# Kernel tuning notes

Measured on AMD Instinct MI355X. Metric: run time of the kernel, lower is better.

The kernel has to match this reference:

```python
import jax, jax.numpy as jnp
import numpy as np

D_MODEL = 1024
D_STATE = 16
EXPAND = 2
D_HEAD = 64
D_CONV = 4
FFN = 2816
NORMALIZE_BC = True
D_INNER = EXPAND * D_MODEL          # 2048
N_HEADS = D_INNER // D_HEAD         # 32
EPS = 1e-6


def _rmsnorm(x, w):
    v = jnp.mean(x * x, axis=-1, keepdims=True)
    return x * jax.lax.rsqrt(v + EPS) * w


def _mixer(x, in_proj_w, conv_w, conv_b, A_log, dt_bias, D, out_proj_w):
    b, l, _ = x.shape
    zxbcdt = x @ in_proj_w.T  # (b, l, 2*D_INNER + 2*D_STATE + N_HEADS)
    z, xBC, dt_raw = jnp.split(zxbcdt, [D_INNER, 2 * D_INNER + 2 * D_STATE], axis=-1)
    # causal depthwise conv over (u, B, C) channels
    xp = jnp.pad(xBC, ((0, 0), (D_CONV - 1, 0), (0, 0)))
    y = conv_b + sum(xp[:, k:k + l, :] * conv_w[:, k] for k in range(D_CONV))
    xBC = jax.nn.silu(y)
    u, Bm, Cm = jnp.split(xBC, [D_INNER, D_INNER + D_STATE], axis=-1)
    if NORMALIZE_BC:
        Bm = Bm / (jnp.linalg.norm(Bm, axis=-1, keepdims=True) + EPS)
        Cm = Cm / (jnp.linalg.norm(Cm, axis=-1, keepdims=True) + EPS)
    dt = jax.nn.softplus(dt_raw + dt_bias)          # (b, l, h)
    A = jnp.exp(A_log)                              # (h, n) oscillator frequencies >= 0
    u = u.reshape(b, l, N_HEADS, D_HEAD)

    # LinOSS implicit (IM) discretization of z' = -A y + B u ; y' = z
    #   S  = 1/(1 + dt^2 A)
    #   w_k = S*(w_{k-1} - dt*A*y_{k-1} + dt*B u_k)
    #   y_k = y_{k-1} + dt*w_k ;  out_k = C y_k + D u_k
    def step(carry, inp):
        w, ys = carry                               # each (b, h, dh, n)
        dt_t, B_t, C_t, u_t = inp                   # (b,h),(b,n),(b,n),(b,h,dh)
        S = 1.0 / (1.0 + (dt_t[:, :, None] ** 2) * A[None])   # (b,h,n)
        Sb = S[:, :, None, :]
        dtb = dt_t[:, :, None, None]
        Ab = A[None, :, None, :]
        Bu = B_t[:, None, None, :] * u_t[..., None]            # (b,h,dh,n)
        w = Sb * (w - dtb * Ab * ys + dtb * Bu)
        ys = ys + dtb * w
        o = jnp.einsum('bhdn,bn->bhd', ys, C_t)
        return (w, ys), o

    init = (jnp.zeros((b, N_HEADS, D_HEAD, D_STATE), x.dtype),
            jnp.zeros((b, N_HEADS, D_HEAD, D_STATE), x.dtype))
    xs = (dt.transpose(1, 0, 2), Bm.transpose(1, 0, 2),
          Cm.transpose(1, 0, 2), u.transpose(1, 0, 2, 3))
    _, ys = jax.lax.scan(step, init, xs)            # (l, b, h, dh)
    ys = ys.transpose(1, 0, 2, 3) + D[None, None, :, None] * u
    out = ys.reshape(b, l, D_INNER) * jax.nn.silu(z)
    return out @ out_proj_w.T


def setup_inputs() -> dict:
    key = jax.random.key(0)
    ks = jax.random.split(key, 12)
    B, L = 4, 2048
    proj_dim = 2 * D_INNER + 2 * D_STATE + N_HEADS
    conv_ch = D_INNER + 2 * D_STATE
    s = lambda k, shape, sc: jax.random.normal(k, shape, jnp.float32) * sc
    return {
        "x": s(ks[0], (B, L, D_MODEL), 1.0),
        "norm1_w": jnp.ones((D_MODEL,), jnp.float32),
        "in_proj_w": s(ks[1], (proj_dim, D_MODEL), D_MODEL ** -0.5),
        "conv_w": s(ks[2], (conv_ch, D_CONV), 0.3),
        "conv_b": jnp.zeros((conv_ch,), jnp.float32),
        "A_log": s(ks[3], (N_HEADS, D_STATE), 0.5),
        "dt_bias": s(ks[4], (N_HEADS,), 0.5),
        "D": s(ks[5], (N_HEADS,), 1.0),
        "out_proj_w": s(ks[6], (D_MODEL, D_INNER), D_INNER ** -0.5),
        "norm2_w": jnp.ones((D_MODEL,), jnp.float32),
        "gate_w": s(ks[7], (FFN, D_MODEL), D_MODEL ** -0.5),
        "up_w": s(ks[8], (FFN, D_MODEL), D_MODEL ** -0.5),
        "down_w": s(ks[9], (D_MODEL, FFN), FFN ** -0.5),
    }


def reference(x, norm1_w, in_proj_w, conv_w, conv_b, A_log, dt_bias, D,
              out_proj_w, norm2_w, gate_w, up_w, down_w):
    h = x + _mixer(_rmsnorm(x, norm1_w), in_proj_w, conv_w, conv_b,
                   A_log, dt_bias, D, out_proj_w)
    hn = _rmsnorm(h, norm2_w)
    ffn = (jax.nn.silu(hn @ gate_w.T) * (hn @ up_w.T)) @ down_w.T
    return h + ffn
```

## Files before the change

kernel.cpp:

```cpp
#include <hip/hip_runtime.h>
#include <hip/hip_bf16.h>

#define D_MODEL   1024
#define D_STATE   16
#define D_HEAD    64
#define D_CONV    4
#define FFN_DIM   2816
#define D_INNER   2048
#define N_HEADS   32
#define BATCH     4
#define SEQ       2048
#define ROWS      (BATCH*SEQ)
#define PROJ_DIM  4160
#define ZX_N      4096
#define CH        128
#define NCH       (SEQ/CH)
#define GU_N      5632

typedef __bf16 bf16x8 __attribute__((ext_vector_type(8)));
typedef float  f32x4  __attribute__((ext_vector_type(4)));
typedef float  f32x2  __attribute__((ext_vector_type(2)));

__device__ __forceinline__ float siluf(float x) { return x / (1.0f + __expf(-x)); }

#define SBAR() do { asm volatile("" ::: "memory"); __builtin_amdgcn_s_barrier(); asm volatile("" ::: "memory"); } while (0)
#define LGKM0() asm volatile("s_waitcnt lgkmcnt(0)" ::: "memory")
#define VMCNT4() asm volatile("s_waitcnt vmcnt(4)" ::: "memory")
#define VMCNT2() asm volatile("s_waitcnt vmcnt(2)" ::: "memory")
#define VMCNT0() asm volatile("s_waitcnt vmcnt(0)" ::: "memory")

__global__ void cvt_k(const float* __restrict__ src, __hip_bfloat16* __restrict__ dst, int n) {
  int i = blockIdx.x * blockDim.x + threadIdx.x;
  if (i < n) dst[i] = __float2bfloat16(src[i]);
}

__global__ void cvt_gu_k(const float* __restrict__ wg, const float* __restrict__ wu,
                         __hip_bfloat16* __restrict__ dst) {
  int i = blockIdx.x * blockDim.x + threadIdx.x;
  if (i >= GU_N * D_MODEL) return;
  int r = i >> 10, c = i & 1023;
  int tile = r >> 8, rr = r & 255;
  const float* src = (rr < 128)
      ? wg + (size_t)(tile * 128 + rr) * D_MODEL + c
      : wu + (size_t)(tile * 128 + (rr - 128)) * D_MODEL + c;
  dst[i] = __float2bfloat16(*src);
}

__global__ __launch_bounds__(256) void rmsnorm_k(const float* __restrict__ x,
                                                 const float* __restrict__ w,
                                                 __hip_bfloat16* __restrict__ out,
                                                 float* __restrict__ outf) {
  int row = blockIdx.x;
  int t = threadIdx.x;
  const float* xr = x + (size_t)row * D_MODEL;
  float4 v = ((const float4*)xr)[t];
  float ss = v.x*v.x + v.y*v.y + v.z*v.z + v.w*v.w;
  #pragma unroll
  for (int o = 32; o > 0; o >>= 1) ss += __shfl_xor(ss, o);
  __shared__ float red[4];
  if ((t & 63) == 0) red[t >> 6] = ss;
  __syncthreads();
  ss = red[0] + red[1] + red[2] + red[3];
  float scale = rsqrtf(ss * (1.0f / D_MODEL) + 1e-6f);
  float4 wv = ((const float4*)w)[t];
  float4 r;
  r.x = v.x * scale * wv.x; r.y = v.y * scale * wv.y;
  r.z = v.z * scale * wv.z; r.w = v.w * scale * wv.w;
  __hip_bfloat16* orow = out + (size_t)row * D_MODEL + t * 4;
  orow[0] = __float2bfloat16(r.x);
  orow[1] = __float2bfloat16(r.y);
  orow[2] = __float2bfloat16(r.z);
  orow[3] = __float2bfloat16(r.w);
  if (outf) ((float4*)(outf + (size_t)row * D_MODEL))[t] = r;
}

__global__ __launch_bounds__(256) void vecproj_k(const float* __restrict__ xn,
                                                 const float* __restrict__ wi,
                                                 const float* __restrict__ dtb,
                                                 float* __restrict__ dtT,
                                                 float* __restrict__ bcraw) {
  const int r0 = blockIdx.x * 4;
  const int t  = threadIdx.x;
  const int o   = t >> 2;
  const int seg = t & 3;

  __shared__ float xs[4][D_MODEL];
  #pragma unroll
  for (int i = 0; i < 4; ++i)
    ((float4*)&xs[i][0])[t] = ((const float4*)(xn + (size_t)(r0 + i) * D_MODEL))[t];
  __syncthreads();

  const int wrow = (o < 32) ? (2 * D_INNER + o) : (2 * D_INNER + 2 * D_STATE + (o - 32));
  const float4* w4 = (const float4*)(wi + (size_t)wrow * D_MODEL) + seg * 64;
  const float4* x0 = (const float4*)&xs[0][0] + seg * 64;
  const float4* x1 = (const float4*)&xs[1][0] + seg * 64;
  const float4* x2 = (const float4*)&xs[2][0] + seg * 64;
  const float4* x3 = (const float4*)&xs[3][0] + seg * 64;
  float a0 = 0.f, a1 = 0.f, a2 = 0.f, a3 = 0.f;
  #pragma unroll 8
  for (int k = 0; k < 64; ++k) {
    float4 wv = w4[k];
    float4 v0 = x0[k], v1 = x1[k], v2 = x2[k], v3 = x3[k];
    a0 = fmaf(wv.x, v0.x, fmaf(wv.y, v0.y, fmaf(wv.z, v0.z, fmaf(wv.w, v0.w, a0))));
    a1 = fmaf(wv.x, v1.x, fmaf(wv.y, v1.y, fmaf(wv.z, v1.z, fmaf(wv.w, v1.w, a1))));
    a2 = fmaf(wv.x, v2.x, fmaf(wv.y, v2.y, fmaf(wv.z, v2.z, fmaf(wv.w, v2.w, a2))));
    a3 = fmaf(wv.x, v3.x, fmaf(wv.y, v3.y, fmaf(wv.z, v3.z, fmaf(wv.w, v3.w, a3))));
  }
  #pragma unroll
  for (int m = 1; m < 4; m <<= 1) {
    a0 += __shfl_xor(a0, m);
    a1 += __shfl_xor(a1, m);
    a2 += __shfl_xor(a2, m);
    a3 += __shfl_xor(a3, m);
  }
  if (seg == 0) {
    float v[4] = {a0, a1, a2, a3};
    if (o < 32) {
      #pragma unroll
      for (int i = 0; i < 4; ++i) bcraw[(size_t)(r0 + i) * 32 + o] = v[i];
    } else {
      int hh = o - 32;
      float bias = dtb[hh];
      #pragma unroll
      for (int i = 0; i < 4; ++i) {
        float xv = v[i] + bias;
        dtT[(size_t)hh * ROWS + r0 + i] = (xv > 20.f) ? xv : log1pf(__expf(xv));
      }
    }
  }
}

template<int EPI>
__global__ __launch_bounds__(512, 2) void gemm8(
    const __hip_bfloat16* __restrict__ A,
    const __hip_bfloat16* __restrict__ Bw,
    float* __restrict__ Cf,
    __hip_bfloat16* __restrict__ Cb,
    const float* __restrict__ add_src,
    int M, int N, int K)
{
  extern __shared__ char lds[];
  const int nwg = (M >> 8) * (N >> 8);
  int bid = blockIdx.x;
  bid = (bid & 7) * (nwg >> 3) + (bid >> 3);
  const int ntn = N >> 8;
  const int bm = (bid / ntn) << 8;
  const int bn = (bid % ntn) << 8;

  const int tid  = threadIdx.x;
  const int wid  = tid >> 6;
  const int lane = tid & 63;
  const int wm = wid >> 2;
  const int wn = wid & 3;
  const int r16 = lane & 15;
  const int kg  = lane >> 4;

  const int rb = ((r16 << 6) + (kg << 4)) ^ ((r16 & 8) << 2);

  const int s_sub = tid >> 6;
  const int s_w   = (tid & 63) << 4;
  const int s_wp  = s_w ^ ((((s_w) >> 9) & 1) << 5);
  const int s_row = ((s_sub >> 1) << 4) + (s_wp >> 6);
  const int s_col = ((s_sub & 1) << 5) + ((s_wp >> 1) & 31);

  auto stage = [&](int buf, int mat, int half, int c, int kt) {
    const __hip_bfloat16* src = (mat == 0)
        ? A  + (size_t)(bm + half * 128 + c * 64 + s_row) * K + kt * 64 + s_col
        : Bw + (size_t)(bn + half * 128 + c * 64 + s_row) * K + kt * 64 + s_col;
    char* dst = lds + buf * 65536 + mat * 32768 + half * 16384 + c * 8192 + tid * 16;
    __builtin_amdgcn_global_load_lds((const __attribute__((address_space(1))) unsigned int*)src,
                                     (__attribute__((address_space(3))) unsigned int*)dst,
                                     16, 0, 0);
  };

  f32x4 acc[8][4] = {};
  bf16x8 af[4][2], bfr[4][2];

  const int NT = K >> 6;
  stage(0,0,0,0,0); stage(0,0,0,1,0); stage(0,0,1,0,0); stage(0,0,1,1,0);
  stage(0,1,0,0,0); stage(0,1,0,1,0); stage(0,1,1,0,0); stage(0,1,1,1,0);
  __syncthreads();

  for (int kt = 0; kt < NT; ++kt) {
    const int buf = kt & 1, nbuf = buf ^ 1;
    const bool st = (kt + 1 < NT);
    const char* Ab = lds + buf * 65536 + wm * 16384;
    const char* Bb = lds + buf * 65536 + 32768 + (wn >> 1) * 16384 + (wn & 1) * 8192;

    #pragma unroll
    for (int mi2 = 0; mi2 < 4; ++mi2)
      #pragma unroll
      for (int kk = 0; kk < 2; ++kk)
        af[mi2][kk] = *(const bf16x8*)(Ab + (mi2 * 2 + kk) * 1024 + rb);
    #pragma unroll
    for (int ni = 0; ni < 2; ++ni)
      #pragma unroll
      for (int kk = 0; kk < 2; ++kk)
        bfr[ni][kk] = *(const bf16x8*)(Bb + (ni * 2 + kk) * 1024 + rb);
    if (st) { stage(nbuf,1,0,0,kt+1); stage(nbuf,1,0,1,kt+1); }
    SBAR(); LGKM0();
    __builtin_amdgcn_s_setprio(1);
    #pragma unroll
    for (int mi2 = 0; mi2 < 4; ++mi2)
      #pragma unroll
      for (int ni = 0; ni < 2; ++ni)
        #pragma unroll
        for (int kk = 0; kk < 2; ++kk)
          acc[mi2][ni] = __builtin_amdgcn_mfma_f32_16x16x32_bf16(af[mi2][kk], bfr[ni][kk], acc[mi2][ni], 0, 0, 0);
    __builtin_amdgcn_s_setprio(0);
    SBAR();

    #pragma unroll
    for (int ni = 2; ni < 4; ++ni)
      #pragma unroll
      for (int kk = 0; kk < 2; ++kk)
        bfr[ni][kk] = *(const bf16x8*)(Bb + (ni * 2 + kk) * 1024 + rb);
    if (st) { stage(nbuf,1,1,0,kt+1); stage(nbuf,1,1,1,kt+1); }
    SBAR(); LGKM0();
    __builtin_amdgcn_s_setprio(1);
    #pragma unroll
    for (int mi2 = 0; mi2 < 4; ++mi2)
      #pragma unroll
      for (int ni = 2; ni < 4; ++ni)
        #pragma unroll
        for (int kk = 0; kk < 2; ++kk)
          acc[mi2][ni] = __builtin_amdgcn_mfma_f32_16x16x32_bf16(af[mi2][kk], bfr[ni][kk], acc[mi2][ni], 0, 0, 0);
    __builtin_amdgcn_s_setprio(0);
    if (st) { VMCNT4(); } else { VMCNT0(); }
    SBAR();

    #pragma unroll
    for (int mi2 = 0; mi2 < 4; ++mi2)
      #pragma unroll
      for (int kk = 0; kk < 2; ++kk)
        af[mi2][kk] = *(const bf16x8*)(Ab + ((4 + mi2) * 2 + kk) * 1024 + rb);
    if (st) { stage(nbuf,0,0,0,kt+1); stage(nbuf,0,1,0,kt+1); }
    SBAR(); LGKM0();
    __builtin_amdgcn_s_setprio(1);
    #pragma unroll
    for (int mi2 = 0; mi2 < 4; ++mi2)
      #pragma unroll
      for (int ni = 0; ni < 2; ++ni)
        #pragma unroll
        for (int kk = 0; kk < 2; ++kk)
          acc[4 + mi2][ni] = __builtin_amdgcn_mfma_f32_16x16x32_bf16(af[mi2][kk], bfr[ni][kk], acc[4 + mi2][ni], 0, 0, 0);
    __builtin_amdgcn_s_setprio(0);
    SBAR();

    if (st) { stage(nbuf,0,0,1,kt+1); stage(nbuf,0,1,1,kt+1); }
    SBAR(); LGKM0();
    __builtin_amdgcn_s_setprio(1);
    #pragma unroll
    for (int mi2 = 0; mi2 < 4; ++mi2)
      #pragma unroll
      for (int ni = 2; ni < 4; ++ni)
        #pragma unroll
        for (int kk = 0; kk < 2; ++kk)
          acc[4 + mi2][ni] = __builtin_amdgcn_mfma_f32_16x16x32_bf16(af[mi2][kk], bfr[ni][kk], acc[4 + mi2][ni], 0, 0, 0);
    __builtin_amdgcn_s_setprio(0);
    VMCNT2();
    SBAR();
  }

  if constexpr (EPI == 4) {
    float* xch = (float*)lds;
    __syncthreads();
    if (wn < 2) {
      #pragma unroll
      for (int mi = 0; mi < 8; ++mi)
        #pragma unroll
        for (int ni = 0; ni < 4; ++ni)
          #pragma unroll
          for (int j = 0; j < 4; ++j) {
            int row = mi * 16 + kg * 4 + j;
            int col = wn * 64 + ni * 16 + r16;
            int cc = col ^ (((row >> 2) & 1) << 4);
            xch[wm * 16384 + row * 128 + cc] = siluf(acc[mi][ni][j]);
          }
    }
    __syncthreads();
    if (wn >= 2) {
      #pragma unroll
      for (int mi = 0; mi < 8; ++mi)
        #pragma unroll
        for (int ni = 0; ni < 4; ++ni)
          #pragma unroll
          for (int j = 0; j < 4; ++j) {
            int row = mi * 16 + kg * 4 + j;
            int col = (wn - 2) * 64 + ni * 16 + r16;
            int cc = col ^ (((row >> 2) & 1) << 4);
            float g = xch[wm * 16384 + row * 128 + cc];
            int r = bm + wm * 128 + row;
            int tc = (bn >> 1) + col;
            Cb[(size_t)r * FFN_DIM + tc] = __float2bfloat16(g * acc[mi][ni][j]);
          }
    }
  } else {
    #pragma unroll
    for (int mi = 0; mi < 8; ++mi) {
      #pragma unroll
      for (int ni = 0; ni < 4; ++ni) {
        #pragma unroll
        for (int j = 0; j < 4; ++j) {
          int r = bm + wm * 128 + mi * 16 + kg * 4 + j;
          int c = bn + wn * 64 + ni * 16 + r16;
          size_t idx = (size_t)r * N + c;
          float v = acc[mi][ni][j];
          if constexpr (EPI == 0) {
            Cf[idx] = v;
          } else if constexpr (EPI == 1) {
            Cf[idx] = v + add_src[idx];
          } else if constexpr (EPI == 5) {
            Cb[idx] = __float2bfloat16(v);
          }
        }
      }
    }
  }
}

template<int EPI>
__global__ __launch_bounds__(512, 2) void gemm8B(
    const __hip_bfloat16* __restrict__ A,
    const __hip_bfloat16* __restrict__ Bw,
    float* __restrict__ Cf,
    __hip_bfloat16* __restrict__ Cb,
    const float* __restrict__ add_src,
    int M, int N, int K)
{
  extern __shared__ char lds[];
  const int nwg = (M >> 8) * (N >> 7);
  int bid = blockIdx.x;
  bid = (bid & 7) * (nwg >> 3) + (bid >> 3);
  const int ntn = N >> 7;
  const int bm = (bid / ntn) << 8;
  const int bn = (bid % ntn) << 7;

  const int tid  = threadIdx.x;
  const int wid  = tid >> 6;
  const int lane = tid & 63;
  const int wm = wid >> 2;
  const int wn = wid & 3;
  const int r16 = lane & 15;
  const int kg  = lane >> 4;

  const int rb = ((r16 << 6) + (kg << 4)) ^ ((r16 & 8) << 2);

  const int s_sub = tid >> 6;
  const int s_w   = (tid & 63) << 4;
  const int s_wp  = s_w ^ ((((s_w) >> 9) & 1) << 5);
  const int s_row = ((s_sub >> 1) << 4) + (s_wp >> 6);
  const int s_col = ((s_sub & 1) << 5) + ((s_wp >> 1) & 31);

  auto stageA = [&](int buf, int half, int c, int kt) {
    const __hip_bfloat16* src = A + (size_t)(bm + half * 128 + c * 64 + s_row) * K + kt * 64 + s_col;
    char* dst = lds + buf * 65536 + half * 16384 + c * 8192 + tid * 16;
    __builtin_amdgcn_global_load_lds((const __attribute__((address_space(1))) unsigned int*)src,
                                     (__attribute__((address_space(3))) unsigned int*)dst,
                                     16, 0, 0);
  };
  auto stageB = [&](int buf, int c, int kt) {
    const __hip_bfloat16* src = Bw + (size_t)(bn + c * 64 + s_row) * K + kt * 64 + s_col;
    char* dst = lds + buf * 65536 + 32768 + c * 8192 + tid * 16;
    __builtin_amdgcn_global_load_lds((const __attribute__((address_space(1))) unsigned int*)src,
                                     (__attribute__((address_space(3))) unsigned int*)dst,
                                     16, 0, 0);
  };

  f32x4 acc[8][2] = {};
  bf16x8 af[4][2], bfr[2][2];

  const int NT = K >> 6;
  stageB(0,0,0); stageB(0,1,0);
  stageA(0,0,0,0); stageA(0,1,0,0); stageA(0,0,1,0); stageA(0,1,1,0);
  __syncthreads();

  for (int kt = 0; kt < NT; ++kt) {
    const int buf = kt & 1, nbuf = buf ^ 1;
    const bool st = (kt + 1 < NT);
    const char* Ab = lds + buf * 65536 + wm * 16384;
    const char* Bb = lds + buf * 65536 + 32768 + (wn >> 1) * 8192 + (wn & 1) * 4096;

    #pragma unroll
    for (int mi2 = 0; mi2 < 4; ++mi2)
      #pragma unroll
      for (int kk = 0; kk < 2; ++kk)
        af[mi2][kk] = *(const bf16x8*)(Ab + (mi2 * 2 + kk) * 1024 + rb);
    #pragma unroll
    for (int ni = 0; ni < 2; ++ni)
      #pragma unroll
      for (int kk = 0; kk < 2; ++kk)
        bfr[ni][kk] = *(const bf16x8*)(Bb + (ni * 2 + kk) * 1024 + rb);
    if (st) { stageB(nbuf,0,kt+1); stageB(nbuf,1,kt+1); stageA(nbuf,0,0,kt+1); stageA(nbuf,1,0,kt+1); }
    SBAR(); LGKM0();
    __builtin_amdgcn_s_setprio(1);
    #pragma unroll
    for (int mi2 = 0; mi2 < 4; ++mi2)
      #pragma unroll
      for (int ni = 0; ni < 2; ++ni)
        #pragma unroll
        for (int kk = 0; kk < 2; ++kk)
          acc[mi2][ni] = __builtin_amdgcn_mfma_f32_16x16x32_bf16(af[mi2][kk], bfr[ni][kk], acc[mi2][ni], 0, 0, 0);
    __builtin_amdgcn_s_setprio(0);
    if (st) { VMCNT4(); } else { VMCNT0(); }
    SBAR();

    #pragma unroll
    for (int mi2 = 0; mi2 < 4; ++mi2)
      #pragma unroll
      for (int kk = 0; kk < 2; ++kk)
        af[mi2][kk] = *(const bf16x8*)(Ab + ((4 + mi2) * 2 + kk) * 1024 + rb);
    if (st) { stageA(nbuf,0,1,kt+1); stageA(nbuf,1,1,kt+1); }
    SBAR(); LGKM0();
    __builtin_amdgcn_s_setprio(1);
    #pragma unroll
    for (int mi2 = 0; mi2 < 4; ++mi2)
      #pragma unroll
      for (int ni = 0; ni < 2; ++ni)
        #pragma unroll
        for (int kk = 0; kk < 2; ++kk)
          acc[4 + mi2][ni] = __builtin_amdgcn_mfma_f32_16x16x32_bf16(af[mi2][kk], bfr[ni][kk], acc[4 + mi2][ni], 0, 0, 0);
    __builtin_amdgcn_s_setprio(0);
    VMCNT2();
    SBAR();
  }

  #pragma unroll
  for (int mi = 0; mi < 8; ++mi) {
    #pragma unroll
    for (int ni = 0; ni < 2; ++ni) {
      #pragma unroll
      for (int j = 0; j < 4; ++j) {
        int r = bm + wm * 128 + mi * 16 + kg * 4 + j;
        int c = bn + wn * 32 + ni * 16 + r16;
        size_t idx = (size_t)r * N + c;
        float v = acc[mi][ni][j];
        if constexpr (EPI == 0) {
          Cf[idx] = v;
        } else if constexpr (EPI == 1) {
          Cf[idx] = v + add_src[idx];
        }
      }
    }
  }
}

__global__ __launch_bounds__(256) void duconv_k(const __hip_bfloat16* __restrict__ zxb,
                                                const float* __restrict__ cw,
                                                const float* __restrict__ cb,
                                                __hip_bfloat16* __restrict__ u_po) {
  int idx = blockIdx.x * 256 + threadIdx.x;
  int q = idx & 511;
  int r = idx >> 9;
  int d0 = q << 2;
  int l = r & (SEQ - 1);
  float4 cb4 = ((const float4*)cb)[q];
  float tw[4][4];
  #pragma unroll
  for (int i = 0; i < 4; ++i) {
    float4 t = ((const float4*)cw)[d0 + i];
    tw[i][0] = t.x; tw[i][1] = t.y; tw[i][2] = t.z; tw[i][3] = t.w;
  }
  float a[4] = {cb4.x, cb4.y, cb4.z, cb4.w};
  #pragma unroll
  for (int k = 0; k < 4; ++k) {
    if (l - 3 + k >= 0) {
      union { ushort4 u4; __hip_bfloat16 b[4]; } R;
      R.u4 = *(const ushort4*)(zxb + (size_t)(r - 3 + k) * ZX_N + D_INNER + d0);
      a[0] = fmaf(__bfloat162float(R.b[0]), tw[0][k], a[0]);
      a[1] = fmaf(__bfloat162float(R.b[1]), tw[1][k], a[1]);
      a[2] = fmaf(__bfloat162float(R.b[2]), tw[2][k], a[2]);
      a[3] = fmaf(__bfloat162float(R.b[3]), tw[3][k], a[3]);
    }
  }
  union { ushort4 u4; __hip_bfloat16 b[4]; } pk;
  #pragma unroll
  for (int i = 0; i < 4; ++i) pk.b[i] = __float2bfloat16(siluf(a[i]));
  *(ushort4*)(u_po + (size_t)r * D_INNER + d0) = pk.u4;
}

__global__ __launch_bounds__(256) void bcdt_k(const float* __restrict__ bcraw,
                                              const float* __restrict__ cw,
                                              const float* __restrict__ cb,
                                              float* __restrict__ bc) {
  int t = threadIdx.x;
  int r = blockIdx.x * 8 + (t >> 5);
  int ch = t & 31;
  int l = r & (SEQ - 1);
  int c = D_INNER + ch;
  float acc = cb[c];
  #pragma unroll
  for (int k = 0; k < 4; ++k) {
    int lp = l - 3 + k;
    if (lp >= 0)
      acc = fmaf(bcraw[(size_t)(r - 3 + k) * 32 + ch], cw[c * 4 + k], acc);
  }
  acc = siluf(acc);
  float ss = acc * acc;
  ss += __shfl_xor(ss, 1);
  ss += __shfl_xor(ss, 2);
  ss += __shfl_xor(ss, 4);
  ss += __shfl_xor(ss, 8);
  bc[r * 32 + ch] = acc / (sqrtf(ss) + 1e-6f);
}

__global__ __launch_bounds__(256) void pk_k(const float* __restrict__ dtT,
                                            const float* __restrict__ A_log,
                                            float* __restrict__ Pm) {
  int bh = blockIdx.x;
  int h = bh & 31;
  int t = threadIdx.x;
  int ch = t >> 4, n = t & 15;
  float a = __expf(A_log[h * 16 + n]);
  const float* dtp = dtT + (size_t)h * ROWS + (size_t)(bh >> 5) * SEQ + ch * CH;
  float p00 = 1.f, p01 = 0.f, p10 = 0.f, p11 = 1.f;
  for (int l = 0; l < CH; ++l) {
    float dt = dtp[l];
    float s  = 1.0f / fmaf(dt * dt, a, 1.0f);
    float m00 = s;
    float m01 = -dt * a * s;
    float m10 = dt * s;
    float m11 = fmaf(-dt * a, m10, 1.0f);
    float q00 = fmaf(m00, p00, m01 * p10);
    float q01 = fmaf(m00, p01, m01 * p11);
    float q10 = fmaf(m10, p00, m11 * p10);
    float q11 = fmaf(m10, p01, m11 * p11);
    p00 = q00; p01 = q01; p10 = q10; p11 = q11;
  }
  float4 v = {p00, p01, p10, p11};
  *(float4*)&Pm[(((size_t)bh * NCH + ch) * 16 + n) * 4] = v;
}

__global__ __launch_bounds__(256) void prop_k(const float* __restrict__ Pm,
                                              const float* __restrict__ pend,
                                              float* __restrict__ sinit) {
  int gid = blockIdx.x * 256 + threadIdx.x;
  int n  = gid & 15;
  int d  = (gid >> 4) & 63;
  int bh = gid >> 10;
  float s0 = 0.f, s1 = 0.f;
  for (int c = 0; c < NCH; ++c) {
    size_t i2 = (((size_t)bh * NCH + c) * 64 + d) * 16 + n;
    *(float2*)&sinit[i2 * 2] = make_float2(s0, s1);
    float4 P  = *(const float4*)&Pm[(((size_t)bh * NCH + c) * 16 + n) * 4];
    float2 pe = *(const float2*)&pend[i2 * 2];
    float t0 = fmaf(P.x, s0, fmaf(P.y, s1, pe.x));
    float t1 = fmaf(P.z, s0, fmaf(P.w, s1, pe.y));
    s0 = t0; s1 = t1;
  }
}

#define T_TILE 16
#define TPC (CH / T_TILE)
template<int PHASE>
__global__ __launch_bounds__(128) void scan_k(
    const __hip_bfloat16* __restrict__ zxb, const float* __restrict__ bcb,
    const float* __restrict__ dtT, const float* __restrict__ A_log,
    const float* __restrict__ Dp, float* __restrict__ states,
    __hip_bfloat16* u_po)
{
  const int blk  = blockIdx.x;
  const int half = blk & 1;
  const int ch   = (blk >> 1) & 15;
  const int h    = (blk >> 5) & 31;
  const int b    = blk >> 10;
  const int bh   = b * 32 + h;
  const int tid  = threadIdx.x;
  const int wv   = tid >> 6;
  const int lane = tid & 63;
  const int d16  = lane & 15;
  const int ng   = lane >> 4;
  const int n0   = ng * 4;
  const int dwv  = wv * 16 + d16;
  const int dl   = half * 32 + dwv;
  const int dbase = h * 64 + half * 32;
  const size_t rowbase = (size_t)b * SEQ + (size_t)ch * CH;

  __shared__ __hip_bfloat16 dut[2][T_TILE][32];
  __shared__ float Btl[2][T_TILE][16];
  __shared__ float Ctl[PHASE == 3 ? 2 : 1][T_TILE][16];
  __shared__ __hip_bfloat16 zt [PHASE == 3 ? 2 : 1][T_TILE][32];
  __shared__ float st [2][T_TILE][16];
  __shared__ float dtt[2][T_TILE];
  __shared__ float aexp[16];
  __shared__ float opart[PHASE == 3 ? T_TILE : 1][32][4];

  if (tid < 16) aexp[tid] = __expf(A_log[h * 16 + tid]);

  f32x2 A2[2];
  #pragma unroll
  for (int k = 0; k < 2; ++k) {
    A2[k][0] = __expf(A_log[h * 16 + n0 + 2 * k]);
    A2[k][1] = __expf(A_log[h * 16 + n0 + 2 * k + 1]);
  }
  const float Dh = Dp[h];

  auto stage = [&](int tile, int buf) {
    const size_t r0 = rowbase + (size_t)tile * T_TILE;
    if constexpr (PHASE == 3) {
      if (wv == 0) {
        const __hip_bfloat16* g = u_po + (r0 + (lane >> 2)) * D_INNER + dbase + (lane & 3) * 8;
        __hip_bfloat16* l_ = &dut[buf][0][0] + lane * 8;
        __builtin_amdgcn_global_load_lds((const __attribute__((address_space(1))) unsigned int*)g,
                                         (__attribute__((address_space(3))) unsigned int*)l_, 16, 0, 0);
      } else {
        const __hip_bfloat16* gz = zxb + (r0 + (lane >> 2)) * ZX_N + dbase + (lane & 3) * 8;
        __hip_bfloat16* lz = &zt[buf][0][0] + lane * 8;
        __builtin_amdgcn_global_load_lds((const __attribute__((address_space(1))) unsigned int*)gz,
                                         (__attribute__((address_space(3))) unsigned int*)lz, 16, 0, 0);
        const float* gB = bcb + (r0 + (lane >> 2)) * 32 + (lane & 3) * 4;
        float* lB = &Btl[buf][0][0] + lane * 4;
        __builtin_amdgcn_global_load_lds((const __attribute__((address_space(1))) unsigned int*)gB,
                                         (__attribute__((address_space(3))) unsigned int*)lB, 16, 0, 0);
        const float* gC = bcb + (r0 + (lane >> 2)) * 32 + 16 + (lane & 3) * 4;
        float* lC = &Ctl[buf][0][0] + lane * 4;
        __builtin_amdgcn_global_load_lds((const __attribute__((address_space(1))) unsigned int*)gC,
                                         (__attribute__((address_space(3))) unsigned int*)lC, 16, 0, 0);
      }
    } else {
      if (wv == 0) {
        const __hip_bfloat16* g = u_po + (r0 + (lane >> 2)) * D_INNER + dbase + (lane & 3) * 8;
        __hip_bfloat16* l_ = &dut[buf][0][0] + lane * 8;
        __builtin_amdgcn_global_load_lds((const __attribute__((address_space(1))) unsigned int*)g,
                                         (__attribute__((address_space(3))) unsigned int*)l_, 16, 0, 0);
      } else {
        const float* gB = bcb + (r0 + (lane >> 2)) * 32 + (lane & 3) * 4;
        float* lB = &Btl[buf][0][0] + lane * 4;
        __builtin_amdgcn_global_load_lds((const __attribute__((address_space(1))) unsigned int*)gB,
                                         (__attribute__((address_space(3))) unsigned int*)lB, 16, 0, 0);
      }
    }
  };

  auto sprep = [&](int buf, float dtn) {
    #pragma unroll
    for (int i = 0; i < 2; ++i) {
      int idx = tid + 128 * i;
      int row = idx >> 4, n = idx & 15;
      float dv = __shfl(dtn, row);
      float a  = aexp[n];
      st[buf][row][n] = 1.0f / fmaf(dv * dv, a, 1.0f);
    }
  };

  stage(0, 0);
  float dtn = 0.f;
  if (lane < 16) dtn = dtT[(size_t)h * ROWS + rowbase + lane];
  __syncthreads();
  if (tid < 16) dtt[0][tid] = dtn;
  sprep(0, dtn);
  __syncthreads();

  f32x2 w2[2], ys2[2];
  if constexpr (PHASE == 1) {
    #pragma unroll
    for (int k = 0; k < 2; ++k) { w2[k] = (f32x2){0.f, 0.f}; ys2[k] = (f32x2){0.f, 0.f}; }
  } else {
    #pragma unroll
    for (int k = 0; k < 2; ++k)
      #pragma unroll
      for (int j = 0; j < 2; ++j) {
        size_t i2 = (((size_t)bh * NCH + ch) * 64 + dl) * 16 + (n0 + 2 * k + j);
        float2 s = *(const float2*)&states[i2 * 2];
        w2[k][j] = s.x; ys2[k][j] = s.y;
      }
  }
  int cur = 0;

  for (int t = 0; t < TPC; ++t) {
    if (t + 1 < TPC) {
      stage(t + 1, cur ^ 1);
      if (lane < 16) dtn = dtT[(size_t)h * ROWS + rowbase + (size_t)(t + 1) * T_TILE + lane];
    }
    #pragma unroll 4
    for (int l = 0; l < T_TILE; ++l) {
      float uv  = __bfloat162float(dut[cur][l][dwv]);
      float dtv = dtt[cur][l];
      f32x4 Sv4 = *(const f32x4*)&st [cur][l][n0];
      f32x4 Bv4 = *(const f32x4*)&Btl[cur][l][n0];
      float du = dtv * uv;
      f32x2 S2[2] = { {Sv4[0], Sv4[1]}, {Sv4[2], Sv4[3]} };
      f32x2 B2[2] = { {Bv4[0], Bv4[1]}, {Bv4[2], Bv4[3]} };
      if constexpr (PHASE == 3) {
        f32x4 Cv4 = *(const f32x4*)&Ctl[cur][l][n0];
        f32x2 C2[2] = { {Cv4[0], Cv4[1]}, {Cv4[2], Cv4[3]} };
        f32x2 o2 = {0.f, 0.f};
        #pragma unroll
        for (int k = 0; k < 2; ++k) {
          f32x2 dtA = dtv * A2[k];
          f32x2 tmp = w2[k] - dtA * ys2[k];
          tmp = tmp + du * B2[k];
          w2[k] = S2[k] * tmp;
          ys2[k] = ys2[k] + dtv * w2[k];
          o2 = o2 + ys2[k] * C2[k];
        }
        float o = o2[0] + o2[1];
        float ofin = (ng == 0) ? fmaf(Dh, uv, o) : o;
        opart[l][dwv][ng] = ofin;
      } else {
        #pragma unroll
        for (int k = 0; k < 2; ++k) {
          f32x2 dtA = dtv * A2[k];
          f32x2 tmp = w2[k] - dtA * ys2[k];
          tmp = tmp + du * B2[k];
          w2[k] = S2[k] * tmp;
          ys2[k] = ys2[k] + dtv * w2[k];
        }
      }
    }
    if constexpr (PHASE == 3) {
      #pragma unroll
      for (int i = 0; i < 4; ++i) {
        int l  = (lane >> 4) + 4 * i;
        int dd = wv * 16 + d16;
        f32x4 op = *(const f32x4*)&opart[l][dd][0];
        float zv = __bfloat162float(zt[cur][l][dd]);
        float yv = (op[0] + op[1]) + (op[2] + op[3]);
        u_po[(rowbase + (size_t)t * T_TILE + l) * D_INNER + dbase + dd] =
            __float2bfloat16(yv * siluf(zv));
      }
    }
    __syncthreads();
    if (t + 1 < TPC) {
      if (tid < 16) dtt[cur ^ 1][tid] = dtn;
      sprep(cur ^ 1, dtn);
      __syncthreads();
    }
    cur ^= 1;
  }

  if constexpr (PHASE == 1) {
    #pragma unroll
    for (int k = 0; k < 2; ++k)
      #pragma unroll
      for (int j = 0; j < 2; ++j) {
        size_t i2 = (((size_t)bh * NCH + ch) * 64 + dl) * 16 + (n0 + 2 * k + j);
        *(float2*)&states[i2 * 2] = make_float2(w2[k][j], ys2[k][j]);
      }
  }
}

extern "C" void kernel_launch(void* const* d_in, const int* in_sizes, int n_in,
                              void* d_out, int out_size, void* d_ws, size_t ws_size,
                              hipStream_t stream) {
  const float* x     = (const float*)d_in[0];
  const float* n1w   = (const float*)d_in[1];
  const float* wi    = (const float*)d_in[2];
  const float* cw    = (const float*)d_in[3];
  const float* cb    = (const float*)d_in[4];
  const float* A_log = (const float*)d_in[5];
  const float* dtb   = (const float*)d_in[6];
  const float* Dp    = (const float*)d_in[7];
  const float* wo    = (const float*)d_in[8];
  const float* n2w   = (const float*)d_in[9];
  const float* wg    = (const float*)d_in[10];
  const float* wu    = (const float*)d_in[11];
  const float* wd    = (const float*)d_in[12];
  float* out = (float*)d_out;

  char* p = (char*)d_ws;
  auto take = [&](size_t b) { char* q = p; p += (b + 255) & ~(size_t)255; return q; };
  __hip_bfloat16* wbi  = (__hip_bfloat16*)take((size_t)ZX_N * D_MODEL * 2);
  __hip_bfloat16* wbo  = (__hip_bfloat16*)take((size_t)D_MODEL * D_INNER * 2);
  __hip_bfloat16* wgu  = (__hip_bfloat16*)take((size_t)GU_N * D_MODEL * 2);
  __hip_bfloat16* wbd  = (__hip_bfloat16*)take((size_t)D_MODEL * FFN_DIM * 2);
  __hip_bfloat16* h0b  = (__hip_bfloat16*)take((size_t)ROWS * D_MODEL * 2);
  char*           region = take((size_t)84 * 1024 * 1024);
  float*          bcb  = (float*)take((size_t)ROWS * 32 * 4);
  float*          bcraw= (float*)take((size_t)ROWS * 32 * 4);
  float*          dtT  = (float*)take((size_t)ROWS * 32 * 4);
  __hip_bfloat16* po   = (__hip_bfloat16*)take((size_t)ROWS * D_INNER * 2);
  float*          pend = (float*)take((size_t)128 * NCH * 64 * 16 * 2 * 4);
  float*          sini = (float*)take((size_t)128 * NCH * 64 * 16 * 2 * 4);
  float*          Pm   = (float*)take((size_t)128 * NCH * 16 * 4 * 4);
  float*          h0f  = (float*)region;
  __hip_bfloat16* zxb  = (__hip_bfloat16*)region;
  float*          h    = (float*)region;
  __hip_bfloat16* gact = (__hip_bfloat16*)(region + 33554432);

  hipFuncSetAttribute(reinterpret_cast<const void*>(&gemm8<5>),  hipFuncAttributeMaxDynamicSharedMemorySize, 131072);
  hipFuncSetAttribute(reinterpret_cast<const void*>(&gemm8<4>),  hipFuncAttributeMaxDynamicSharedMemorySize, 131072);
  hipFuncSetAttribute(reinterpret_cast<const void*>(&gemm8B<1>), hipFuncAttributeMaxDynamicSharedMemorySize, 131072);

  cvt_k<<<(ZX_N * D_MODEL + 255) / 256, 256, 0, stream>>>(wi, wbi, ZX_N * D_MODEL);
  cvt_k<<<(D_MODEL * D_INNER + 255) / 256, 256, 0, stream>>>(wo, wbo, D_MODEL * D_INNER);
  cvt_gu_k<<<(GU_N * D_MODEL + 255) / 256, 256, 0, stream>>>(wg, wu, wgu);
  cvt_k<<<(FFN_DIM * D_MODEL + 255) / 256, 256, 0, stream>>>(wd, wbd, FFN_DIM * D_MODEL);

  rmsnorm_k<<<ROWS, 256, 0, stream>>>(x, n1w, h0b, h0f);
  vecproj_k<<<ROWS / 4, 256, 0, stream>>>(h0f, wi, dtb, dtT, bcraw);
  gemm8<5><<<(ROWS / 256) * (ZX_N / 256), 512, 131072, stream>>>(h0b, wbi, nullptr, zxb, nullptr,
                                                                 ROWS, ZX_N, D_MODEL);
  duconv_k<<<ROWS * 512 / 256, 256, 0, stream>>>(zxb, cw, cb, po);
  bcdt_k<<<ROWS / 8, 256, 0, stream>>>(bcraw, cw, cb, bcb);
  pk_k<<<BATCH * N_HEADS, 256, 0, stream>>>(dtT, A_log, Pm);
  scan_k<1><<<BATCH * N_HEADS * NCH * 2, 128, 0, stream>>>(zxb, bcb, dtT, A_log, Dp, pend, po);
  prop_k<<<BATCH * N_HEADS * 64 * 16 / 256, 256, 0, stream>>>(Pm, pend, sini);
  scan_k<3><<<BATCH * N_HEADS * NCH * 2, 128, 0, stream>>>(zxb, bcb, dtT, A_log, Dp, sini, po);
  gemm8B<1><<<(ROWS / 256) * (D_MODEL / 128), 512, 131072, stream>>>(po, wbo, h, nullptr, x,
                                                                     ROWS, D_MODEL, D_INNER);
  rmsnorm_k<<<ROWS, 256, 0, stream>>>(h, n2w, h0b, nullptr);
  gemm8<4><<<(ROWS / 256) * (GU_N / 256), 512, 131072, stream>>>(h0b, wgu, nullptr, gact, nullptr,
                                                                 ROWS, GU_N, D_MODEL);
  gemm8B<1><<<(ROWS / 256) * (D_MODEL / 128), 512, 131072, stream>>>(gact, wbd, out, nullptr, h,
                                                                     ROWS, D_MODEL, FFN_DIM);
}
```

Before: 606.8 us.

## Replace 256x256 GEMM with smaller 256x128, K=32 tile kernel at higher occupancy

Replaces the large 256x256-tile, K=64 double-buffered GEMM used for the input projection and the gate/up projection with a 256x128-tile, K=32 kernel that uses 48KB of LDS and launch bounds allowing 4 blocks per CU. The gate/up weight interleave changes to 64-row groups to match the narrower tile, and the SiLU exchange in the epilogue now goes through bf16 LDS. The goal is more resident blocks and a simpler single-phase loop with fewer barriers. The cost is lower arithmetic intensity per tile, twice as many K iterations, and a full vmcnt(0) wait on every iteration, which removes the earlier fine-grained overlap.

```diff
diff --git a/kernel.cpp b/kernel.cpp
--- a/kernel.cpp
+++ b/kernel.cpp
@@ -39,10 +39,10 @@
   int i = blockIdx.x * blockDim.x + threadIdx.x;
   if (i >= GU_N * D_MODEL) return;
   int r = i >> 10, c = i & 1023;
-  int tile = r >> 8, rr = r & 255;
-  const float* src = (rr < 128)
-      ? wg + (size_t)(tile * 128 + rr) * D_MODEL + c
-      : wu + (size_t)(tile * 128 + (rr - 128)) * D_MODEL + c;
+  int tile = r >> 7, rr = r & 127;
+  const float* src = (rr < 64)
+      ? wg + (size_t)(tile * 64 + rr) * D_MODEL + c
+      : wu + (size_t)(tile * 64 + (rr - 64)) * D_MODEL + c;
   dst[i] = __float2bfloat16(*src);
 }
 
@@ -131,27 +131,25 @@
 }
 
 template<int EPI>
-__global__ __launch_bounds__(512, 2) void gemm8(
+__global__ __launch_bounds__(512, 4) void gemmT(
     const __hip_bfloat16* __restrict__ A,
     const __hip_bfloat16* __restrict__ Bw,
-    float* __restrict__ Cf,
     __hip_bfloat16* __restrict__ Cb,
-    const float* __restrict__ add_src,
     int M, int N, int K)
 {
   extern __shared__ char lds[];
-  const int nwg = (M >> 8) * (N >> 8);
+  const int nwg = (M >> 8) * (N >> 7);
   int bid = blockIdx.x;
   bid = (bid & 7) * (nwg >> 3) + (bid >> 3);
-  const int ntn = N >> 8;
+  const int ntn = N >> 7;
   const int bm = (bid / ntn) << 8;
-  const int bn = (bid % ntn) << 8;
+  const int bn = (bid % ntn) << 7;
 
   const int tid  = threadIdx.x;
   const int wid  = tid >> 6;
   const int lane = tid & 63;
-  const int wm = wid >> 2;
-  const int wn = wid & 3;
+  const int wm = wid >> 1;
+  const int wn = wid & 1;
   const int r16 = lane & 15;
   const int kg  = lane >> 4;
 
@@ -160,162 +158,94 @@
   const int s_sub = tid >> 6;
   const int s_w   = (tid & 63) << 4;
   const int s_wp  = s_w ^ ((((s_w) >> 9) & 1) << 5);
-  const int s_row = ((s_sub >> 1) << 4) + (s_wp >> 6);
-  const int s_col = ((s_sub & 1) << 5) + ((s_wp >> 1) & 31);
-
-  auto stage = [&](int buf, int mat, int half, int c, int kt) {
-    const __hip_bfloat16* src = (mat == 0)
-        ? A  + (size_t)(bm + half * 128 + c * 64 + s_row) * K + kt * 64 + s_col
-        : Bw + (size_t)(bn + half * 128 + c * 64 + s_row) * K + kt * 64 + s_col;
-    char* dst = lds + buf * 65536 + mat * 32768 + half * 16384 + c * 8192 + tid * 16;
+  const int s_row = (s_sub << 4) + (s_wp >> 6);
+  const int s_col = (s_wp >> 1) & 31;
+
+  auto stageA = [&](int buf, int h, int kt) {
+    const __hip_bfloat16* src = A + (size_t)(bm + h * 128 + s_row) * K + kt * 32 + s_col;
+    char* dst = lds + buf * 24576 + h * 8192 + tid * 16;
     __builtin_amdgcn_global_load_lds((const __attribute__((address_space(1))) unsigned int*)src,
                                      (__attribute__((address_space(3))) unsigned int*)dst,
                                      16, 0, 0);
   };
-
-  f32x4 acc[8][4] = {};
-  bf16x8 af[4][2], bfr[4][2];
-
-  const int NT = K >> 6;
-  stage(0,0,0,0,0); stage(0,0,0,1,0); stage(0,0,1,0,0); stage(0,0,1,1,0);
-  stage(0,1,0,0,0); stage(0,1,0,1,0); stage(0,1,1,0,0); stage(0,1,1,1,0);
+  auto stageB = [&](int buf, int kt) {
+    const __hip_bfloat16* src = Bw + (size_t)(bn + s_row) * K + kt * 32 + s_col;
+    char* dst = lds + buf * 24576 + 16384 + tid * 16;
+    __builtin_amdgcn_global_load_lds((const __attribute__((address_space(1))) unsigned int*)src,
+                                     (__attribute__((address_space(3))) unsigned int*)dst,
+                                     16, 0, 0);
+  };
+
+  f32x4 acc[4][4] = {};
+
+  const int NT = K >> 5;
+  stageA(0, 0, 0); stageA(0, 1, 0); stageB(0, 0);
   __syncthreads();
 
   for (int kt = 0; kt < NT; ++kt) {
     const int buf = kt & 1, nbuf = buf ^ 1;
     const bool st = (kt + 1 < NT);
-    const char* Ab = lds + buf * 65536 + wm * 16384;
-    const char* Bb = lds + buf * 65536 + 32768 + (wn >> 1) * 16384 + (wn & 1) * 8192;
-
-    #pragma unroll
-    for (int mi2 = 0; mi2 < 4; ++mi2)
-      #pragma unroll
-      for (int kk = 0; kk < 2; ++kk)
-        af[mi2][kk] = *(const bf16x8*)(Ab + (mi2 * 2 + kk) * 1024 + rb);
-    #pragma unroll
-    for (int ni = 0; ni < 2; ++ni)
-      #pragma unroll
-      for (int kk = 0; kk < 2; ++kk)
-        bfr[ni][kk] = *(const bf16x8*)(Bb + (ni * 2 + kk) * 1024 + rb);
-    if (st) { stage(nbuf,1,0,0,kt+1); stage(nbuf,1,0,1,kt+1); }
-    SBAR(); LGKM0();
+    const char* Ab = lds + buf * 24576 + wm * 4096;
+    const char* Bb = lds + buf * 24576 + 16384 + wn * 4096;
+
+    bf16x8 af[4], bfr[4];
+    #pragma unroll
+    for (int mi = 0; mi < 4; ++mi) af[mi]  = *(const bf16x8*)(Ab + mi * 1024 + rb);
+    #pragma unroll
+    for (int ni = 0; ni < 4; ++ni) bfr[ni] = *(const bf16x8*)(Bb + ni * 1024 + rb);
+    if (st) { stageA(nbuf, 0, kt + 1); stageA(nbuf, 1, kt + 1); stageB(nbuf, kt + 1); }
     __builtin_amdgcn_s_setprio(1);
     #pragma unroll
-    for (int mi2 = 0; mi2 < 4; ++mi2)
-      #pragma unroll
-      for (int ni = 0; ni < 2; ++ni)
-        #pragma unroll
-        for (int kk = 0; kk < 2; ++kk)
-          acc[mi2][ni] = __builtin_amdgcn_mfma_f32_16x16x32_bf16(af[mi2][kk], bfr[ni][kk], acc[mi2][ni], 0, 0, 0);
+    for (int mi = 0; mi < 4; ++mi)
+      #pragma unroll
+      for (int ni = 0; ni < 4; ++ni)
+        acc[mi][ni] = __builtin_amdgcn_mfma_f32_16x16x32_bf16(af[mi], bfr[ni], acc[mi][ni], 0, 0, 0);
     __builtin_amdgcn_s_setprio(0);
+    VMCNT0();
     SBAR();
-
-    #pragma unroll
-    for (int ni = 2; ni < 4; ++ni)
-      #pragma unroll
-      for (int kk = 0; kk < 2; ++kk)
-        bfr[ni][kk] = *(const bf16x8*)(Bb + (ni * 2 + kk) * 1024 + rb);
-    if (st) { stage(nbuf,1,1,0,kt+1); stage(nbuf,1,1,1,kt+1); }
-    SBAR(); LGKM0();
-    __builtin_amdgcn_s_setprio(1);
-    #pragma unroll
-    for (int mi2 = 0; mi2 < 4; ++mi2)
-      #pragma unroll
-      for (int ni = 2; ni < 4; ++ni)
-        #pragma unroll
-        for (int kk = 0; kk < 2; ++kk)
-          acc[mi2][ni] = __builtin_amdgcn_mfma_f32_16x16x32_bf16(af[mi2][kk], bfr[ni][kk], acc[mi2][ni], 0, 0, 0);
-    __builtin_amdgcn_s_setprio(0);
-    if (st) { VMCNT4(); } else { VMCNT0(); }
-    SBAR();
-
-    #pragma unroll
-    for (int mi2 = 0; mi2 < 4; ++mi2)
-      #pragma unroll
-      for (int kk = 0; kk < 2; ++kk)
-        af[mi2][kk] = *(const bf16x8*)(Ab + ((4 + mi2) * 2 + kk) * 1024 + rb);
-    if (st) { stage(nbuf,0,0,0,kt+1); stage(nbuf,0,1,0,kt+1); }
-    SBAR(); LGKM0();
-    __builtin_amdgcn_s_setprio(1);
-    #pragma unroll
-    for (int mi2 = 0; mi2 < 4; ++mi2)
-      #pragma unroll
-      for (int ni = 0; ni < 2; ++ni)
-        #pragma unroll
-        for (int kk = 0; kk < 2; ++kk)
-          acc[4 + mi2][ni] = __builtin_amdgcn_mfma_f32_16x16x32_bf16(af[mi2][kk], bfr[ni][kk], acc[4 + mi2][ni], 0, 0, 0);
-    __builtin_amdgcn_s_setprio(0);
-    SBAR();
-
-    if (st) { stage(nbuf,0,0,1,kt+1); stage(nbuf,0,1,1,kt+1); }
-    SBAR(); LGKM0();
-    __builtin_amdgcn_s_setprio(1);
-    #pragma unroll
-    for (int mi2 = 0; mi2 < 4; ++mi2)
-      #pragma unroll
-      for (int ni = 2; ni < 4; ++ni)
-        #pragma unroll
-        for (int kk = 0; kk < 2; ++kk)
-          acc[4 + mi2][ni] = __builtin_amdgcn_mfma_f32_16x16x32_bf16(af[mi2][kk], bfr[ni][kk], acc[4 + mi2][ni], 0, 0, 0);
-    __builtin_amdgcn_s_setprio(0);
-    VMCNT2();
-    SBAR();
   }
 
   if constexpr (EPI == 4) {
-    float* xch = (float*)lds;
+    __hip_bfloat16* xch = (__hip_bfloat16*)lds;
     __syncthreads();
-    if (wn < 2) {
-      #pragma unroll
-      for (int mi = 0; mi < 8; ++mi)
+    if (wn == 0) {
+      #pragma unroll
+      for (int mi = 0; mi < 4; ++mi)
         #pragma unroll
         for (int ni = 0; ni < 4; ++ni)
           #pragma unroll
           for (int j = 0; j < 4; ++j) {
-            int row = mi * 16 + kg * 4 + j;
-            int col = wn * 64 + ni * 16 + r16;
-            int cc = col ^ (((row >> 2) & 1) << 4);
-            xch[wm * 16384 + row * 128 + cc] = siluf(acc[mi][ni][j]);
+            int row = wm * 64 + mi * 16 + kg * 4 + j;
+            int col = ni * 16 + r16;
+            xch[row * 72 + col] = __float2bfloat16(siluf(acc[mi][ni][j]));
           }
     }
     __syncthreads();
-    if (wn >= 2) {
-      #pragma unroll
-      for (int mi = 0; mi < 8; ++mi)
+    if (wn == 1) {
+      #pragma unroll
+      for (int mi = 0; mi < 4; ++mi)
         #pragma unroll
         for (int ni = 0; ni < 4; ++ni)
           #pragma unroll
           for (int j = 0; j < 4; ++j) {
-            int row = mi * 16 + kg * 4 + j;
-            int col = (wn - 2) * 64 + ni * 16 + r16;
-            int cc = col ^ (((row >> 2) & 1) << 4);
-            float g = xch[wm * 16384 + row * 128 + cc];
-            int r = bm + wm * 128 + row;
-            int tc = (bn >> 1) + col;
-            Cb[(size_t)r * FFN_DIM + tc] = __float2bfloat16(g * acc[mi][ni][j]);
+            int row = wm * 64 + mi * 16 + kg * 4 + j;
+            int col = ni * 16 + r16;
+            float g = __bfloat162float(xch[row * 72 + col]);
+            Cb[(size_t)(bm + row) * FFN_DIM + (bn >> 1) + col] =
+                __float2bfloat16(g * acc[mi][ni][j]);
           }
     }
   } else {
     #pragma unroll
-    for (int mi = 0; mi < 8; ++mi) {
-      #pragma unroll
-      for (int ni = 0; ni < 4; ++ni) {
+    for (int mi = 0; mi < 4; ++mi)
+      #pragma unroll
+      for (int ni = 0; ni < 4; ++ni)
         #pragma unroll
         for (int j = 0; j < 4; ++j) {
-          int r = bm + wm * 128 + mi * 16 + kg * 4 + j;
+          int r = bm + wm * 64 + mi * 16 + kg * 4 + j;
           int c = bn + wn * 64 + ni * 16 + r16;
-          size_t idx = (size_t)r * N + c;
-          float v = acc[mi][ni][j];
-          if constexpr (EPI == 0) {
-            Cf[idx] = v;
-          } else if constexpr (EPI == 1) {
-            Cf[idx] = v + add_src[idx];
-          } else if constexpr (EPI == 5) {
-            Cb[idx] = __float2bfloat16(v);
-          }
+          Cb[(size_t)r * N + c] = __float2bfloat16(acc[mi][ni][j]);
         }
-      }
-    }
   }
 }
 
@@ -778,8 +708,8 @@
   float*          h    = (float*)region;
   __hip_bfloat16* gact = (__hip_bfloat16*)(region + 33554432);
 
-  hipFuncSetAttribute(reinterpret_cast<const void*>(&gemm8<5>),  hipFuncAttributeMaxDynamicSharedMemorySize, 131072);
-  hipFuncSetAttribute(reinterpret_cast<const void*>(&gemm8<4>),  hipFuncAttributeMaxDynamicSharedMemorySize, 131072);
+  hipFuncSetAttribute(reinterpret_cast<const void*>(&gemmT<5>),  hipFuncAttributeMaxDynamicSharedMemorySize, 49152);
+  hipFuncSetAttribute(reinterpret_cast<const void*>(&gemmT<4>),  hipFuncAttributeMaxDynamicSharedMemorySize, 49152);
   hipFuncSetAttribute(reinterpret_cast<const void*>(&gemm8B<1>), hipFuncAttributeMaxDynamicSharedMemorySize, 131072);
 
   cvt_k<<<(ZX_N * D_MODEL + 255) / 256, 256, 0, stream>>>(wi, wbi, ZX_N * D_MODEL);
@@ -789,8 +719,8 @@
 
   rmsnorm_k<<<ROWS, 256, 0, stream>>>(x, n1w, h0b, h0f);
   vecproj_k<<<ROWS / 4, 256, 0, stream>>>(h0f, wi, dtb, dtT, bcraw);
-  gemm8<5><<<(ROWS / 256) * (ZX_N / 256), 512, 131072, stream>>>(h0b, wbi, nullptr, zxb, nullptr,
-                                                                 ROWS, ZX_N, D_MODEL);
+  gemmT<5><<<(ROWS / 256) * (ZX_N / 128), 512, 49152, stream>>>(h0b, wbi, zxb,
+                                                                ROWS, ZX_N, D_MODEL);
   duconv_k<<<ROWS * 512 / 256, 256, 0, stream>>>(zxb, cw, cb, po);
   bcdt_k<<<ROWS / 8, 256, 0, stream>>>(bcraw, cw, cb, bcb);
   pk_k<<<BATCH * N_HEADS, 256, 0, stream>>>(dtT, A_log, Pm);
@@ -800,8 +730,8 @@
   gemm8B<1><<<(ROWS / 256) * (D_MODEL / 128), 512, 131072, stream>>>(po, wbo, h, nullptr, x,
                                                                      ROWS, D_MODEL, D_INNER);
   rmsnorm_k<<<ROWS, 256, 0, stream>>>(h, n2w, h0b, nullptr);
-  gemm8<4><<<(ROWS / 256) * (GU_N / 256), 512, 131072, stream>>>(h0b, wgu, nullptr, gact, nullptr,
-                                                                 ROWS, GU_N, D_MODEL);
+  gemmT<4><<<(ROWS / 256) * (GU_N / 128), 512, 49152, stream>>>(h0b, wgu, gact,
+                                                                ROWS, GU_N, D_MODEL);
   gemm8B<1><<<(ROWS / 256) * (D_MODEL / 128), 512, 131072, stream>>>(gact, wbd, out, nullptr, h,
                                                                      ROWS, D_MODEL, FFN_DIM);
 }
```

Result: slower. 623.8 us (+2.8%).

## Use smaller-tile gemmT kernel for fused gate/up FFN GEMM

Applied to the files above, without the earlier changes.

Adds a new gemmT kernel with 256x128 tiles, 48KB LDS, double buffering and launch bounds allowing four blocks per CU, and uses it for the fused gate/up projection. The gate/up weight interleave shrinks from 128-row to 64-row halves to match the narrower tile. The silu-gate exchange in LDS now stores bf16 instead of fp32. The goal is higher occupancy and better load balance across CUs, at the cost of less reuse per tile and a simpler pipeline.

```diff
diff --git a/kernel.cpp b/kernel.cpp
--- a/kernel.cpp
+++ b/kernel.cpp
@@ -39,10 +39,10 @@
   int i = blockIdx.x * blockDim.x + threadIdx.x;
   if (i >= GU_N * D_MODEL) return;
   int r = i >> 10, c = i & 1023;
-  int tile = r >> 8, rr = r & 255;
-  const float* src = (rr < 128)
-      ? wg + (size_t)(tile * 128 + rr) * D_MODEL + c
-      : wu + (size_t)(tile * 128 + (rr - 128)) * D_MODEL + c;
+  int tile = r >> 7, rr = r & 127;
+  const float* src = (rr < 64)
+      ? wg + (size_t)(tile * 64 + rr) * D_MODEL + c
+      : wu + (size_t)(tile * 64 + (rr - 64)) * D_MODEL + c;
   dst[i] = __float2bfloat16(*src);
 }
 
@@ -134,9 +134,7 @@
 __global__ __launch_bounds__(512, 2) void gemm8(
     const __hip_bfloat16* __restrict__ A,
     const __hip_bfloat16* __restrict__ Bw,
-    float* __restrict__ Cf,
     __hip_bfloat16* __restrict__ Cb,
-    const float* __restrict__ add_src,
     int M, int N, int K)
 {
   extern __shared__ char lds[];
@@ -262,60 +260,136 @@
     SBAR();
   }
 
+  #pragma unroll
+  for (int mi = 0; mi < 8; ++mi) {
+    #pragma unroll
+    for (int ni = 0; ni < 4; ++ni) {
+      #pragma unroll
+      for (int j = 0; j < 4; ++j) {
+        int r = bm + wm * 128 + mi * 16 + kg * 4 + j;
+        int c = bn + wn * 64 + ni * 16 + r16;
+        Cb[(size_t)r * N + c] = __float2bfloat16(acc[mi][ni][j]);
+      }
+    }
+  }
+}
+
+template<int EPI>
+__global__ __launch_bounds__(512, 4) void gemmT(
+    const __hip_bfloat16* __restrict__ A,
+    const __hip_bfloat16* __restrict__ Bw,
+    __hip_bfloat16* __restrict__ Cb,
+    int M, int N, int K)
+{
+  extern __shared__ char lds[];
+  const int nwg = (M >> 8) * (N >> 7);
+  int bid = blockIdx.x;
+  bid = (bid & 7) * (nwg >> 3) + (bid >> 3);
+  const int ntn = N >> 7;
+  const int bm = (bid / ntn) << 8;
+  const int bn = (bid % ntn) << 7;
+
+  const int tid  = threadIdx.x;
+  const int wid  = tid >> 6;
+  const int lane = tid & 63;
+  const int wm = wid >> 1;
+  const int wn = wid & 1;
+  const int r16 = lane & 15;
+  const int kg  = lane >> 4;
+
+  const int rb = ((r16 << 6) + (kg << 4)) ^ ((r16 & 8) << 2);
+
+  const int s_sub = tid >> 6;
+  const int s_w   = (tid & 63) << 4;
+  const int s_wp  = s_w ^ ((((s_w) >> 9) & 1) << 5);
+  const int s_row = (s_sub << 4) + (s_wp >> 6);
+  const int s_col = (s_wp >> 1) & 31;
+
+  auto stageA = [&](int buf, int h, int kt) {
+    const __hip_bfloat16* src = A + (size_t)(bm + h * 128 + s_row) * K + kt * 32 + s_col;
+    char* dst = lds + buf * 24576 + h * 8192 + tid * 16;
+    __builtin_amdgcn_global_load_lds((const __attribute__((address_space(1))) unsigned int*)src,
+                                     (__attribute__((address_space(3))) unsigned int*)dst,
+                                     16, 0, 0);
+  };
+  auto stageB = [&](int buf, int kt) {
+    const __hip_bfloat16* src = Bw + (size_t)(bn + s_row) * K + kt * 32 + s_col;
+    char* dst = lds + buf * 24576 + 16384 + tid * 16;
+    __builtin_amdgcn_global_load_lds((const __attribute__((address_space(1))) unsigned int*)src,
+                                     (__attribute__((address_space(3))) unsigned int*)dst,
+                                     16, 0, 0);
+  };
+
+  f32x4 acc[4][4] = {};
+
+  const int NT = K >> 5;
+  stageA(0, 0, 0); stageA(0, 1, 0); stageB(0, 0);
+  __syncthreads();
+
+  for (int kt = 0; kt < NT; ++kt) {
+    const int buf = kt & 1, nbuf = buf ^ 1;
+    const bool st = (kt + 1 < NT);
+    const char* Ab = lds + buf * 24576 + wm * 4096;
+    const char* Bb = lds + buf * 24576 + 16384 + wn * 4096;
+
+    bf16x8 af[4], bfr[4];
+    #pragma unroll
+    for (int mi = 0; mi < 4; ++mi) af[mi]  = *(const bf16x8*)(Ab + mi * 1024 + rb);
+    #pragma unroll
+    for (int ni = 0; ni < 4; ++ni) bfr[ni] = *(const bf16x8*)(Bb + ni * 1024 + rb);
+    if (st) { stageA(nbuf, 0, kt + 1); stageA(nbuf, 1, kt + 1); stageB(nbuf, kt + 1); }
+    __builtin_amdgcn_s_setprio(1);
+    #pragma unroll
+    for (int mi = 0; mi < 4; ++mi)
+      #pragma unroll
+      for (int ni = 0; ni < 4; ++ni)
+        acc[mi][ni] = __builtin_amdgcn_mfma_f32_16x16x32_bf16(af[mi], bfr[ni], acc[mi][ni], 0, 0, 0);
+    __builtin_amdgcn_s_setprio(0);
+    VMCNT0();
+    SBAR();
+  }
+
   if constexpr (EPI == 4) {
-    float* xch = (float*)lds;
+    __hip_bfloat16* xch = (__hip_bfloat16*)lds;
     __syncthreads();
-    if (wn < 2) {
-      #pragma unroll
-      for (int mi = 0; mi < 8; ++mi)
+    if (wn == 0) {
+      #pragma unroll
+      for (int mi = 0; mi < 4; ++mi)
         #pragma unroll
         for (int ni = 0; ni < 4; ++ni)
           #pragma unroll
           for (int j = 0; j < 4; ++j) {
-            int row = mi * 16 + kg * 4 + j;
-            int col = wn * 64 + ni * 16 + r16;
-            int cc = col ^ (((row >> 2) & 1) << 4);
-            xch[wm * 16384 + row * 128 + cc] = siluf(acc[mi][ni][j]);
+            int row = wm * 64 + mi * 16 + kg * 4 + j;
+            int col = ni * 16 + r16;
+            xch[row * 72 + col] = __float2bfloat16(siluf(acc[mi][ni][j]));
           }
     }
     __syncthreads();
-    if (wn >= 2) {
-      #pragma unroll
-      for (int mi = 0; mi < 8; ++mi)
+    if (wn == 1) {
+      #pragma unroll
+      for (int mi = 0; mi < 4; ++mi)
         #pragma unroll
         for (int ni = 0; ni < 4; ++ni)
           #pragma unroll
           for (int j = 0; j < 4; ++j) {
-            int row = mi * 16 + kg * 4 + j;
-            int col = (wn - 2) * 64 + ni * 16 + r16;
-            int cc = col ^ (((row >> 2) & 1) << 4);
-            float g = xch[wm * 16384 + row * 128 + cc];
-            int r = bm + wm * 128 + row;
-            int tc = (bn >> 1) + col;
-            Cb[(size_t)r * FFN_DIM + tc] = __float2bfloat16(g * acc[mi][ni][j]);
+            int row = wm * 64 + mi * 16 + kg * 4 + j;
+            int col = ni * 16 + r16;
+            float g = __bfloat162float(xch[row * 72 + col]);
+            Cb[(size_t)(bm + row) * FFN_DIM + (bn >> 1) + col] =
+                __float2bfloat16(g * acc[mi][ni][j]);
           }
     }
   } else {
     #pragma unroll
-    for (int mi = 0; mi < 8; ++mi) {
-      #pragma unroll
-      for (int ni = 0; ni < 4; ++ni) {
+    for (int mi = 0; mi < 4; ++mi)
+      #pragma unroll
+      for (int ni = 0; ni < 4; ++ni)
         #pragma unroll
         for (int j = 0; j < 4; ++j) {
-          int r = bm + wm * 128 + mi * 16 + kg * 4 + j;
+          int r = bm + wm * 64 + mi * 16 + kg * 4 + j;
           int c = bn + wn * 64 + ni * 16 + r16;
-          size_t idx = (size_t)r * N + c;
-          float v = acc[mi][ni][j];
-          if constexpr (EPI == 0) {
-            Cf[idx] = v;
-          } else if constexpr (EPI == 1) {
-            Cf[idx] = v + add_src[idx];
-          } else if constexpr (EPI == 5) {
-            Cb[idx] = __float2bfloat16(v);
-          }
+          Cb[(size_t)r * N + c] = __float2bfloat16(acc[mi][ni][j]);
         }
-      }
-    }
   }
 }
 
@@ -779,7 +853,7 @@
   __hip_bfloat16* gact = (__hip_bfloat16*)(region + 33554432);
 
   hipFuncSetAttribute(reinterpret_cast<const void*>(&gemm8<5>),  hipFuncAttributeMaxDynamicSharedMemorySize, 131072);
-  hipFuncSetAttribute(reinterpret_cast<const void*>(&gemm8<4>),  hipFuncAttributeMaxDynamicSharedMemorySize, 131072);
+  hipFuncSetAttribute(reinterpret_cast<const void*>(&gemmT<4>),  hipFuncAttributeMaxDynamicSharedMemorySize, 49152);
   hipFuncSetAttribute(reinterpret_cast<const void*>(&gemm8B<1>), hipFuncAttributeMaxDynamicSharedMemorySize, 131072);
 
   cvt_k<<<(ZX_N * D_MODEL + 255) / 256, 256, 0, stream>>>(wi, wbi, ZX_N * D_MODEL);
@@ -789,7 +863,7 @@
 
   rmsnorm_k<<<ROWS, 256, 0, stream>>>(x, n1w, h0b, h0f);
   vecproj_k<<<ROWS / 4, 256, 0, stream>>>(h0f, wi, dtb, dtT, bcraw);
-  gemm8<5><<<(ROWS / 256) * (ZX_N / 256), 512, 131072, stream>>>(h0b, wbi, nullptr, zxb, nullptr,
+  gemm8<5><<<(ROWS / 256) * (ZX_N / 256), 512, 131072, stream>>>(h0b, wbi, zxb,
                                                                  ROWS, ZX_N, D_MODEL);
   duconv_k<<<ROWS * 512 / 256, 256, 0, stream>>>(zxb, cw, cb, po);
   bcdt_k<<<ROWS / 8, 256, 0, stream>>>(bcraw, cw, cb, bcb);
@@ -800,8 +874,8 @@
   gemm8B<1><<<(ROWS / 256) * (D_MODEL / 128), 512, 131072, stream>>>(po, wbo, h, nullptr, x,
                                                                      ROWS, D_MODEL, D_INNER);
   rmsnorm_k<<<ROWS, 256, 0, stream>>>(h, n2w, h0b, nullptr);
-  gemm8<4><<<(ROWS / 256) * (GU_N / 256), 512, 131072, stream>>>(h0b, wgu, nullptr, gact, nullptr,
-                                                                 ROWS, GU_N, D_MODEL);
+  gemmT<4><<<(ROWS / 256) * (GU_N / 128), 512, 49152, stream>>>(h0b, wgu, gact,
+                                                                ROWS, GU_N, D_MODEL);
   gemm8B<1><<<(ROWS / 256) * (D_MODEL / 128), 512, 131072, stream>>>(gact, wbd, out, nullptr, h,
                                                                      ROWS, D_MODEL, FFN_DIM);
 }
```

Measured after the change: 602.5 us. About the same (-0.7%).
